# Optimization experiments

Measured on AMD Instinct MI355X. Metric: run time of the kernel, lower is better.

Reference implementation:

```python
import jax, jax.numpy as jnp
import numpy as np

N_QUBITS = 12
R = 1
EDGES = [(i, (i + 1) % N_QUBITS) for i in range(N_QUBITS)]
DIM = 2 ** N_QUBITS
BATCH = 64
_LET = 'abcdefghijklmnopqrstuvwxy'

_I4 = np.eye(4, dtype=np.float32)
_AD = np.fliplr(_I4).copy()                      # antidiagonal (XX imag pattern)
_YP = np.array([[0,0,0,1],[0,0,-1,0],[0,-1,0,0],[1,0,0,0]], dtype=np.float32)  # YY imag pattern
_CNOT = jnp.asarray(np.array([[1,0,0,0],[0,1,0,0],[0,0,0,1],[0,0,1,0]], dtype=np.complex64))
_k = np.arange(DIM)
# z_signs[i, k] = -1 if bit (n-i-1) of k is set, matching the torch buffer
_ZS = jnp.asarray(np.stack([1.0 - 2.0 * ((_k >> (N_QUBITS - i - 1)) & 1) for i in range(N_QUBITS)]).astype(np.float32))  # [n, 2^n]


def _c(r, i):
    return jax.lax.complex(r, i)


def rx_mat(t):
    c, s, z = jnp.cos(t / 2), jnp.sin(t / 2), jnp.zeros_like(t)
    real = jnp.stack([jnp.stack([c, z], -1), jnp.stack([z, c], -1)], -2)
    imag = jnp.stack([jnp.stack([z, -s], -1), jnp.stack([-s, z], -1)], -2)
    return _c(real, imag)


def ry_mat(t):
    c, s = jnp.cos(t / 2), jnp.sin(t / 2)
    real = jnp.stack([jnp.stack([c, -s], -1), jnp.stack([s, c], -1)], -2)
    return _c(real, jnp.zeros_like(real))


def rz_mat(t):
    p, z = t / 2, jnp.zeros_like(t)
    cp, sp = jnp.cos(p), jnp.sin(p)
    real = jnp.stack([jnp.stack([cp, z], -1), jnp.stack([z, cp], -1)], -2)
    imag = jnp.stack([jnp.stack([-sp, z], -1), jnp.stack([z, sp], -1)], -2)
    return _c(real, imag)


def ising_zz(t):
    p = t / 2
    c, s = jnp.cos(p), jnp.sin(p)
    dr = jnp.stack([c, c, c, c], -1)
    di = jnp.stack([-s, s, s, -s], -1)
    i4 = jnp.asarray(_I4)
    return _c(dr[..., :, None] * i4, di[..., :, None] * i4)


def ising_xx(t):
    c, s = jnp.cos(t / 2), jnp.sin(t / 2)
    return _c(c[..., None, None] * jnp.asarray(_I4), -s[..., None, None] * jnp.asarray(_AD))


def ising_yy(t):
    c, s = jnp.cos(t / 2), jnp.sin(t / 2)
    return _c(c[..., None, None] * jnp.asarray(_I4), s[..., None, None] * jnp.asarray(_YP))


def apply_1q(state, gate, q):
    # state [B, 2^n]; gate [2,2] or [B,2,2]; qubit axis sits at stride 2^q (matches torch view)
    B = state.shape[0]
    left, right = 2 ** (N_QUBITS - q - 1), 2 ** q
    s = state.reshape(B, left, 2, right)
    sub = 'bij' if gate.ndim == 3 else 'ij'
    return jnp.einsum(f'{sub},bljr->blir', gate, s).reshape(B, DIM)


def apply_2q(state, gate, q1, q2):
    # state [B, 2^n]; gate [4,4]; qubit index = tensor-axis index from MSB (matches torch permute path)
    if q1 > q2:
        q1, q2 = q2, q1
    B = state.shape[0]
    s = state.reshape((B,) + (2,) * N_QUBITS)
    g = gate.reshape(2, 2, 2, 2)
    ax = list(_LET[:N_QUBITS])
    out = ax.copy()
    u, v = ax[q1], ax[q2]
    out[q1], out[q2] = 'A', 'B'
    spec = f"AB{u}{v},Z{''.join(ax)}->Z{''.join(out)}"
    return jnp.einsum(spec, g, s).reshape(B, DIM)


def _forward(data, encoding_scale, encoding_bias, eta, ew_zz, ew_xx, ew_yy, nb_z, nb_x, nb_y, trainable_rots):
    B, n = data.shape
    # data-encoding gates, cached once per forward: angles [B, n] -> gates [B, n, 2, 2]
    rx_g = rx_mat(encoding_scale[:, 0] * data + encoding_bias[:, 0])
    ry_g = ry_mat(encoding_scale[:, 1] * data + encoding_bias[:, 1])
    rz_g = rz_mat(encoding_scale[:, 2] * data + encoding_bias[:, 2])
    state = jnp.zeros((B, DIM), jnp.complex64).at[:, 0].set(1.0)
    ising_fns = (ising_zz, ising_xx, ising_yy)
    ews = (ew_zz, ew_xx, ew_yy)
    nbs = (nb_z, nb_x, nb_y)
    bias_fns = (rz_mat, rx_mat, ry_mat)
    enc_types = ('full', 'xy', 'yz')
    for r in range(R):
        for b in range(3):  # blocks: ZZ, XX, YY
            bt = enc_types[b]
            # data encoding
            for q in range(n):
                if bt != 'yz':
                    state = apply_1q(state, rx_g[:, q], q)
                state = apply_1q(state, ry_g[:, q], q)
                if bt != 'xy':
                    state = apply_1q(state, rz_g[:, q], q)
            # Ising interaction on each edge
            theta = eta[r, b] * ews[b][r]            # [n_edges]
            egs = ising_fns[b](theta)                # [n_edges, 4, 4]
            for e, (i, j) in enumerate(EDGES):
                state = apply_2q(state, egs[e], i, j)
            # node biases (RZ / RX / RY matching the block)
            bgs = bias_fns[b](nbs[b][r])             # [n, 2, 2]
            for q in range(n):
                state = apply_1q(state, bgs[q], q)
            # trainable rotations rx, ry, rz per qubit
            rots = trainable_rots[r, b]              # [n, 3]
            rxg, ryg, rzg = rx_mat(rots[:, 0]), ry_mat(rots[:, 1]), rz_mat(rots[:, 2])
            for q in range(n):
                state = apply_1q(state, rxg[q], q)
                state = apply_1q(state, ryg[q], q)
                state = apply_1q(state, rzg[q], q)
            # CNOT entangling ring
            for q in range(n):
                state = apply_2q(state, _CNOT, q, (q + 1) % n)
    probs = state.real ** 2 + state.imag ** 2        # [B, 2^n]
    return probs @ _ZS.T                             # Pauli-Z expectations [B, n]


def setup_inputs() -> dict:
    key = jax.random.key(0)
    ks = jax.random.split(key, 12)
    n, E, f = N_QUBITS, len(EDGES), jnp.float32
    return {
        'data': jax.random.uniform(ks[0], (BATCH, n), f),
        'encoding_scale': jnp.pi * jnp.ones((n, 3), f) + 0.1 * jax.random.normal(ks[1], (n, 3), f),
        'encoding_bias': 0.1 * jax.random.normal(ks[2], (n, 3), f),
        'eta': 0.5 * jnp.ones((R, 3), f),
        'ew_zz': jnp.ones((R, E), f) + 0.1 * jax.random.normal(ks[3], (R, E), f),
        'ew_xx': jnp.ones((R, E), f) + 0.1 * jax.random.normal(ks[4], (R, E), f),
        'ew_yy': jnp.ones((R, E), f) + 0.1 * jax.random.normal(ks[5], (R, E), f),
        'nb_z': 0.1 * jax.random.normal(ks[6], (R, n), f),
        'nb_x': 0.1 * jax.random.normal(ks[7], (R, n), f),
        'nb_y': 0.1 * jax.random.normal(ks[8], (R, n), f),
        'trainable_rots': 0.1 * jax.random.normal(ks[9], (R, 3, n, 3), f),
    }


def reference(data, encoding_scale, encoding_bias, eta, ew_zz, ew_xx, ew_yy, nb_z, nb_x, nb_y, trainable_rots):
    return _forward(data, encoding_scale, encoding_bias, eta, ew_zz, ew_xx, ew_yy, nb_z, nb_x, nb_y, trainable_rots)
```

## Files before the change

### kernel.cpp

```cpp
#include <hip/hip_runtime.h>
#include <math.h>

#define NT 512
#define QDIM 4096

using F2 = float2;

__device__ __forceinline__ F2 cadd(F2 p, F2 q) { return make_float2(p.x + q.x, p.y + q.y); }
__device__ __forceinline__ F2 cmul(F2 p, F2 q) {
    return make_float2(p.x * q.x - p.y * q.y, p.x * q.y + p.y * q.x);
}

struct M2 { F2 a, b, c, d; };

__device__ __forceinline__ M2 mmul(M2 A, M2 B) {
    M2 R;
    R.a = cadd(cmul(A.a, B.a), cmul(A.b, B.c));
    R.b = cadd(cmul(A.a, B.b), cmul(A.b, B.d));
    R.c = cadd(cmul(A.c, B.a), cmul(A.d, B.c));
    R.d = cadd(cmul(A.c, B.b), cmul(A.d, B.d));
    return R;
}

__device__ __forceinline__ M2 mrx(float t) {
    float s, c; sincosf(0.5f * t, &s, &c);
    return { make_float2(c, 0), make_float2(0, -s), make_float2(0, -s), make_float2(c, 0) };
}
__device__ __forceinline__ M2 mry(float t) {
    float s, c; sincosf(0.5f * t, &s, &c);
    return { make_float2(c, 0), make_float2(-s, 0), make_float2(s, 0), make_float2(c, 0) };
}
__device__ __forceinline__ M2 mrz(float t) {
    float s, c; sincosf(0.5f * t, &s, &c);
    return { make_float2(c, -s), make_float2(0, 0), make_float2(0, 0), make_float2(c, s) };
}

#define RSQ2 0.70710678118654752f
__device__ __forceinline__ M2 mH() {
    return { make_float2(RSQ2, 0), make_float2(RSQ2, 0), make_float2(RSQ2, 0), make_float2(-RSQ2, 0) };
}
__device__ __forceinline__ M2 mW() {
    return { make_float2(RSQ2, 0), make_float2(0, RSQ2), make_float2(RSQ2, 0), make_float2(0, -RSQ2) };
}
__device__ __forceinline__ M2 mWd() {
    return { make_float2(RSQ2, 0), make_float2(RSQ2, 0), make_float2(0, -RSQ2), make_float2(0, RSQ2) };
}


template<int Li>
__device__ __forceinline__ int kOf(int t, int j) {
    const int mlo = (1 << (3 * Li)) - 1;
    return (t & mlo) | (j << (3 * Li)) | ((t & ~mlo) << 3);
}
template<int Li>
__device__ __forceinline__ int slotOf(int k) {
    const int mlo = (1 << (3 * Li)) - 1;
    int j = (k >> (3 * Li)) & 7;
    int t = (k & mlo) | ((k >> 3) & ~mlo);
    return j * 512 + (t ^ j);
}

template<int LA, int LB>
__device__ __forceinline__ void trip(F2* amp, int tid, F2* b) {
#pragma unroll
    for (int j = 0; j < 8; ++j) b[j * 512 + (tid ^ j)] = amp[j];
    __syncthreads();
#pragma unroll
    for (int j = 0; j < 8; ++j) amp[j] = b[slotOf<LA>(kOf<LB>(tid, j))];
}

template<int JB>
__device__ __forceinline__ void g1_reg(F2* amp, const F2* g) {
    const int m = 1 << JB;
    F2 m00 = g[0], m01 = g[1], m10 = g[2], m11 = g[3];
#pragma unroll
    for (int j = 0; j < 8; ++j)
        if (!(j & m)) {
            F2 a = amp[j], b = amp[j | m];
            amp[j]     = cadd(cmul(m00, a), cmul(m01, b));
            amp[j | m] = cadd(cmul(m10, a), cmul(m11, b));
        }
}

__device__ __forceinline__ void diag_L3(F2* amp, const float* zh, int tid) {
    float phi0 = 0.f;
#pragma unroll
    for (int e = 3; e <= 10; ++e) {
        int hi = 11 - e, lo = 10 - e;
        phi0 += (((tid >> hi) ^ (tid >> lo)) & 1) ? zh[e] : -zh[e];
    }
    float z0 = zh[0], z1 = zh[1], z2 = zh[2], z11 = zh[11];
    int t8 = (tid >> 8) & 1, t0 = tid & 1;
#pragma unroll
    for (int j = 0; j < 8; ++j) {
        int j0 = j & 1, j1 = (j >> 1) & 1, j2 = (j >> 2) & 1;
        float phi = phi0
            + ((j2 ^ j1) ? z0 : -z0)
            + ((j1 ^ j0) ? z1 : -z1)
            + ((j0 ^ t8) ? z2 : -z2)
            + ((j2 ^ t0) ? z11 : -z11);
        float sp, cp;
        __sincosf(phi, &sp, &cp);
        amp[j] = cmul(amp[j], make_float2(cp, sp));
    }
}

__device__ __forceinline__ int cnot_src(int k) {
#pragma unroll
    for (int e = 11; e >= 0; --e) {
        int hi = (e < 11) ? 11 - e : 11, lo = (e < 11) ? 10 - e : 0;
        if ((k >> hi) & 1) k ^= (1 << lo);
    }
    return k;
}

__device__ __forceinline__ void cnot_trip(F2* amp, int tid, const int* kslot, F2* b) {
#pragma unroll
    for (int j = 0; j < 8; ++j) b[j * 512 + (tid ^ j)] = amp[j];
    __syncthreads();
#pragma unroll
    for (int j = 0; j < 8; ++j) amp[j] = b[kslot[j]];
}

__global__ __launch_bounds__(NT) void qsim_kernel(
    const float* __restrict__ data,
    const float* __restrict__ enc_scale,
    const float* __restrict__ enc_bias,
    const float* __restrict__ eta,
    const float* __restrict__ ew_zz,
    const float* __restrict__ ew_xx,
    const float* __restrict__ ew_yy,
    const float* __restrict__ nb_z,
    const float* __restrict__ nb_x,
    const float* __restrict__ nb_y,
    const float* __restrict__ trots,
    float* __restrict__ out)
{
    __shared__ F2 buf[2][QDIM];
    __shared__ F2 g1q[72][4];
    __shared__ float zhalf[3][12];
    __shared__ float red[8][12];

    const int tid = threadIdx.x;
    const int bat = blockIdx.x;

    if (tid < 36) {
        int b = tid / 12, q = tid % 12;
        float x  = data[bat * 12 + q];
        float ax = enc_scale[q * 3 + 0] * x + enc_bias[q * 3 + 0];
        float ay = enc_scale[q * 3 + 1] * x + enc_bias[q * 3 + 1];
        float az = enc_scale[q * 3 + 2] * x + enc_bias[q * 3 + 2];
        M2 M;
        if (b == 0)      M = mmul(mrz(az), mmul(mry(ay), mrx(ax)));
        else if (b == 1) M = mmul(mH(), mmul(mry(ay), mrx(ax)));
        else             M = mmul(mW(), mmul(mrz(az), mry(ay)));
        g1q[tid][0] = M.a; g1q[tid][1] = M.b; g1q[tid][2] = M.c; g1q[tid][3] = M.d;
    } else if (tid < 72) {
        int i = tid - 36, b = i / 12, q = i % 12;
        float nb = (b == 0) ? nb_z[q] : (b == 1) ? nb_x[q] : nb_y[q];
        M2 M0 = (b == 0) ? mrz(nb) : (b == 1) ? mrx(nb) : mry(nb);
        float t0 = trots[(b * 12 + q) * 3 + 0];
        float t1 = trots[(b * 12 + q) * 3 + 1];
        float t2 = trots[(b * 12 + q) * 3 + 2];
        M2 M = mmul(mrz(t2), mmul(mry(t1), mmul(mrx(t0), M0)));
        if (b == 1)      M = mmul(M, mH());
        else if (b == 2) M = mmul(M, mWd());
        g1q[tid][0] = M.a; g1q[tid][1] = M.b; g1q[tid][2] = M.c; g1q[tid][3] = M.d;
    } else if (tid < 108) {
        int i = tid - 72, b = i / 12, e = i % 12;
        const float* ew = (b == 0) ? ew_zz : (b == 1) ? ew_xx : ew_yy;
        zhalf[b][e] = 0.5f * eta[b] * ew[e];
    }
    __syncthreads();

    F2 amp[8];
#pragma unroll
    for (int j = 0; j < 8; ++j) amp[j] = make_float2(0.f, 0.f);
    if (tid == 0) amp[0].x = 1.f;

    int kslot[8];
#pragma unroll
    for (int j = 0; j < 8; ++j)
        kslot[j] = slotOf<0>(cnot_src(kOf<0>(tid, j)));

    int sel = 0;
#define NB (&buf[(sel ^= 1) ^ 1][0])

    for (int blk = 0; blk < 3; ++blk) {
        const F2(*Ge)[4] = &g1q[blk * 12];
        const F2(*Gb)[4] = &g1q[36 + blk * 12];

        g1_reg<0>(amp, Ge[0]);  g1_reg<1>(amp, Ge[1]);  g1_reg<2>(amp, Ge[2]);
        trip<0,1>(amp, tid, NB);
        g1_reg<0>(amp, Ge[3]);  g1_reg<1>(amp, Ge[4]);  g1_reg<2>(amp, Ge[5]);
        trip<1,2>(amp, tid, NB);
        g1_reg<0>(amp, Ge[6]);  g1_reg<1>(amp, Ge[7]);  g1_reg<2>(amp, Ge[8]);
        trip<2,3>(amp, tid, NB);
        g1_reg<0>(amp, Ge[9]);  g1_reg<1>(amp, Ge[10]); g1_reg<2>(amp, Ge[11]);

        diag_L3(amp, zhalf[blk], tid);

        g1_reg<0>(amp, Gb[9]);  g1_reg<1>(amp, Gb[10]); g1_reg<2>(amp, Gb[11]);
        trip<3,2>(amp, tid, NB);
        g1_reg<0>(amp, Gb[6]);  g1_reg<1>(amp, Gb[7]);  g1_reg<2>(amp, Gb[8]);
        trip<2,1>(amp, tid, NB);
        g1_reg<0>(amp, Gb[3]);  g1_reg<1>(amp, Gb[4]);  g1_reg<2>(amp, Gb[5]);
        trip<1,0>(amp, tid, NB);
        g1_reg<0>(amp, Gb[0]);  g1_reg<1>(amp, Gb[1]);  g1_reg<2>(amp, Gb[2]);

        cnot_trip(amp, tid, kslot, NB);
    }

    float pr[8];
#pragma unroll
    for (int j = 0; j < 8; ++j) pr[j] = amp[j].x * amp[j].x + amp[j].y * amp[j].y;
    float psum = 0.f;
#pragma unroll
    for (int j = 0; j < 8; ++j) psum += pr[j];

    float acc[12];
#pragma unroll
    for (int i = 0; i < 9; ++i)
        acc[i] = ((tid >> (8 - i)) & 1) ? -psum : psum;
#pragma unroll
    for (int i = 9; i < 12; ++i) {
        float s = 0.f;
        int bit = 11 - i;
#pragma unroll
        for (int j = 0; j < 8; ++j)
            s += ((j >> bit) & 1) ? -pr[j] : pr[j];
        acc[i] = s;
    }
#pragma unroll
    for (int off = 32; off > 0; off >>= 1)
#pragma unroll
        for (int i = 0; i < 12; ++i)
            acc[i] += __shfl_down(acc[i], off, 64);
    int wv = tid >> 6;
    if ((tid & 63) == 0)
#pragma unroll
        for (int i = 0; i < 12; ++i) red[wv][i] = acc[i];
    __syncthreads();
    if (tid < 12) {
        float s = 0.f;
#pragma unroll
        for (int ww = 0; ww < 8; ++ww) s += red[ww][tid];
        out[bat * 12 + tid] = s;
    }
}

extern "C" void kernel_launch(void* const* d_in, const int* in_sizes, int n_in,
                              void* d_out, int out_size, void* d_ws, size_t ws_size,
                              hipStream_t stream) {
    const float* data      = (const float*)d_in[0];
    const float* enc_scale = (const float*)d_in[1];
    const float* enc_bias  = (const float*)d_in[2];
    const float* eta       = (const float*)d_in[3];
    const float* ew_zz     = (const float*)d_in[4];
    const float* ew_xx     = (const float*)d_in[5];
    const float* ew_yy     = (const float*)d_in[6];
    const float* nb_z      = (const float*)d_in[7];
    const float* nb_x      = (const float*)d_in[8];
    const float* nb_y      = (const float*)d_in[9];
    const float* trots     = (const float*)d_in[10];
    float* out = (float*)d_out;

    int batch = out_size / 12;
    qsim_kernel<<<batch, NT, 0, stream>>>(data, enc_scale, enc_bias, eta,
                                          ew_zz, ew_xx, ew_yy,
                                          nb_z, nb_x, nb_y, trots, out);
}
```

Baseline: 103.3 us.

## Use wave-local shared-memory transposes to avoid block barriers for low qubits

Four of the six qubit-group transposes per block now run within a single wavefront through a per-wave scratch region, with no __syncthreads. This is possible because the low 9 qubits (bits within a 64-lane wave times 8 registers) stay inside one wave. The remaining two are block-wide transposes with a simplified index mapping. The goal is to cut block barriers and address arithmetic, at the cost of an extra 32KB of LDS, which may reduce occupancy. Wave-local correctness depends on in-order LDS execution within a wave, and only a compiler memory barrier is used between the store and load phases.

```diff
diff --git a/kernel.cpp b/kernel.cpp
--- a/kernel.cpp
+++ b/kernel.cpp
@@ -52,21 +52,31 @@
     const int mlo = (1 << (3 * Li)) - 1;
     return (t & mlo) | (j << (3 * Li)) | ((t & ~mlo) << 3);
 }
-template<int Li>
-__device__ __forceinline__ int slotOf(int k) {
-    const int mlo = (1 << (3 * Li)) - 1;
-    int j = (k >> (3 * Li)) & 7;
-    int t = (k & mlo) | ((k >> 3) & ~mlo);
+__device__ __forceinline__ int slot0(int k) {
+    int j = k & 7, t = k >> 3;
     return j * 512 + (t ^ j);
 }
 
-template<int LA, int LB>
-__device__ __forceinline__ void trip(F2* amp, int tid, F2* b) {
+template<int TYPE>
+__device__ __forceinline__ void itrip(F2* amp, int l, F2* wb) {
+#pragma unroll
+    for (int j = 0; j < 8; ++j) wb[j * 64 + (l ^ ((9 * j) & 63))] = amp[j];
+    asm volatile("" ::: "memory");
+#pragma unroll
+    for (int j = 0; j < 8; ++j) {
+        int jo, lo;
+        if (TYPE == 0) { jo = l & 7;        lo = j | (l & 56); }
+        else           { jo = (l >> 3) & 7; lo = (l & 7) | (j << 3); }
+        amp[j] = wb[jo * 64 + (lo ^ ((9 * jo) & 63))];
+    }
+}
+
+__device__ __forceinline__ void btrip(F2* amp, int tid, int l, int wv, F2* b) {
 #pragma unroll
     for (int j = 0; j < 8; ++j) b[j * 512 + (tid ^ j)] = amp[j];
     __syncthreads();
 #pragma unroll
-    for (int j = 0; j < 8; ++j) amp[j] = b[slotOf<LA>(kOf<LB>(tid, j))];
+    for (int j = 0; j < 8; ++j) amp[j] = b[wv * 512 + ((j * 64 + l) ^ wv)];
 }
 
 template<int JB>
@@ -136,13 +146,16 @@
     const float* __restrict__ trots,
     float* __restrict__ out)
 {
-    __shared__ F2 buf[2][QDIM];
+    __shared__ F2 bbuf[2][QDIM];
+    __shared__ F2 ibuf[QDIM];
     __shared__ F2 g1q[72][4];
     __shared__ float zhalf[3][12];
     __shared__ float red[8][12];
 
     const int tid = threadIdx.x;
+    const int l = tid & 63, wv = tid >> 6;
     const int bat = blockIdx.x;
+    F2* wb = &ibuf[wv * 512];
 
     if (tid < 36) {
         int b = tid / 12, q = tid % 12;
@@ -181,31 +194,31 @@
     int kslot[8];
 #pragma unroll
     for (int j = 0; j < 8; ++j)
-        kslot[j] = slotOf<0>(cnot_src(kOf<0>(tid, j)));
+        kslot[j] = slot0(cnot_src(kOf<0>(tid, j)));
 
     int sel = 0;
-#define NB (&buf[(sel ^= 1) ^ 1][0])
+#define NB (&bbuf[(sel ^= 1) ^ 1][0])
 
     for (int blk = 0; blk < 3; ++blk) {
         const F2(*Ge)[4] = &g1q[blk * 12];
         const F2(*Gb)[4] = &g1q[36 + blk * 12];
 
         g1_reg<0>(amp, Ge[0]);  g1_reg<1>(amp, Ge[1]);  g1_reg<2>(amp, Ge[2]);
-        trip<0,1>(amp, tid, NB);
+        itrip<0>(amp, l, wb);
         g1_reg<0>(amp, Ge[3]);  g1_reg<1>(amp, Ge[4]);  g1_reg<2>(amp, Ge[5]);
-        trip<1,2>(amp, tid, NB);
+        itrip<1>(amp, l, wb);
         g1_reg<0>(amp, Ge[6]);  g1_reg<1>(amp, Ge[7]);  g1_reg<2>(amp, Ge[8]);
-        trip<2,3>(amp, tid, NB);
+        btrip(amp, tid, l, wv, NB);
         g1_reg<0>(amp, Ge[9]);  g1_reg<1>(amp, Ge[10]); g1_reg<2>(amp, Ge[11]);
 
         diag_L3(amp, zhalf[blk], tid);
 
         g1_reg<0>(amp, Gb[9]);  g1_reg<1>(amp, Gb[10]); g1_reg<2>(amp, Gb[11]);
-        trip<3,2>(amp, tid, NB);
+        btrip(amp, tid, l, wv, NB);
         g1_reg<0>(amp, Gb[6]);  g1_reg<1>(amp, Gb[7]);  g1_reg<2>(amp, Gb[8]);
-        trip<2,1>(amp, tid, NB);
+        itrip<1>(amp, l, wb);
         g1_reg<0>(amp, Gb[3]);  g1_reg<1>(amp, Gb[4]);  g1_reg<2>(amp, Gb[5]);
-        trip<1,0>(amp, tid, NB);
+        itrip<0>(amp, l, wb);
         g1_reg<0>(amp, Gb[0]);  g1_reg<1>(amp, Gb[1]);  g1_reg<2>(amp, Gb[2]);
 
         cnot_trip(amp, tid, kslot, NB);
@@ -236,7 +249,6 @@
 #pragma unroll
         for (int i = 0; i < 12; ++i)
             acc[i] += __shfl_down(acc[i], off, 64);
-    int wv = tid >> 6;
     if ((tid & 63) == 0)
 #pragma unroll
         for (int i = 0; i < 12; ++i) red[wv][i] = acc[i];
```

Result: faster. 100.3 us (-2.9%).
